# Performance work log

Hardware: AMD Instinct MI355X
Metric: run time of the kernel (lower is better)

## Reference

```python
import jax, jax.numpy as jnp
import numpy as np

H = 256  # hidden_size


def setup_inputs() -> dict:
    key = jax.random.key(0)
    ks = jax.random.split(key, 9)
    std = 1.0 / np.sqrt(H)
    u = lambda k, shape: jax.random.uniform(k, shape, jnp.float32, -std, std)
    x = jax.random.normal(ks[0], (64, 16, 128, 64), jnp.float32)
    return {
        "x": x,
        "wi0": u(ks[1], (64, 3 * H)),
        "wh0": u(ks[2], (H, 3 * H)),
        "bi0": u(ks[3], (3 * H,)),
        "bh0": u(ks[4], (3 * H,)),
        "wi1": u(ks[5], (H, 3 * H)),
        "wh1": u(ks[6], (H, 3 * H)),
        "bi1": u(ks[7], (3 * H,)),
        "bh1": u(ks[8], (3 * H,)),
    }


def _cell(x_t, h, wi, wh, bi, bh):
    # x_t: (B, N, D), h: (B, N, H). Gates concatenated as [r|z|n].
    gi = x_t @ wi + bi           # (B, N, 3H)
    gh = h @ wh + bh             # (B, N, 3H)
    ir, iz, inn = jnp.split(gi, 3, axis=-1)
    hr, hz, hn = jnp.split(gh, 3, axis=-1)
    r = jax.nn.sigmoid(ir + hr)
    z = jax.nn.sigmoid(iz + hz)
    n = jnp.tanh(inn + r * hn)
    return (1.0 - z) * n + z * h


def reference(x, wi0, wh0, bi0, bh0, wi1, wh1, bi1, bh1):
    seq_len, B, N, _ = x.shape
    h0 = jnp.zeros((B, N, H), x.dtype)
    h1 = jnp.zeros((B, N, H), x.dtype)

    def step(carry, x_t):
        h0, h1 = carry
        h0 = _cell(x_t, h0, wi0, wh0, bi0, bh0)
        h1 = _cell(h0, h1, wi1, wh1, bi1, bh1)
        return (h0, h1), h1

    (h0, h1), output = jax.lax.scan(step, (h0, h1), x)
    hidden_out = jnp.stack([h0, h1], axis=0)  # (num_layers, B, N, H)
    return output, hidden_out
```

## Files before the change

kernel.cpp:

```cpp
#include <hip/hip_runtime.h>


typedef __attribute__((ext_vector_type(8))) __bf16 bf8;
typedef __attribute__((ext_vector_type(8))) unsigned short u16x8;
typedef __attribute__((ext_vector_type(4))) float f32x4;

#define MFMA16(A, B, C) __builtin_amdgcn_mfma_f32_16x16x32_bf16((A), (B), (C), 0, 0, 0)

#define ROWS 2048
#define HID 256
#define NW 768
#define SLOT (ROWS * HID)
#define OUT_HID_OFF ((size_t)64 * ROWS * HID)

#define WI1_OFF 0
#define WH1_OFF 12288

static __device__ __forceinline__ float b2f(unsigned short u) {
  union { unsigned u32; float f; } v;
  v.u32 = ((unsigned)u) << 16;
  return v.f;
}
static __device__ __forceinline__ unsigned short f2b(float f) {
  unsigned u = __float_as_uint(f);
  u += 0x7fffu + ((u >> 16) & 1u);
  return (unsigned short)(u >> 16);
}
static __device__ __forceinline__ float sigm(float x) {
  return 1.0f / (1.0f + __expf(-x));
}
static __device__ __forceinline__ float tanh_fast(float x) {
  x = fminf(15.0f, fmaxf(-15.0f, x));
  float e = __expf(2.0f * x);
  return (e - 1.0f) / (e + 1.0f);
}
static __device__ __forceinline__ float ldin(const void* p, int i, int f32w) {
  return f32w ? ((const float*)p)[i] : b2f(((const unsigned short*)p)[i]);
}
static __device__ __forceinline__ void stout(void* p, size_t i, float v, int f32w) {
  if (f32w) ((float*)p)[i] = v;
  else ((unsigned short*)p)[i] = f2b(v);
}

static __device__ __forceinline__ bf8 ld_h16(const unsigned short* p) {
  union { unsigned long long q[2]; bf8 b; } u;
  u.q[0] = __hip_atomic_load((const unsigned long long*)p, __ATOMIC_RELAXED,
                             __HIP_MEMORY_SCOPE_AGENT);
  u.q[1] = __hip_atomic_load((const unsigned long long*)(p + 4), __ATOMIC_RELAXED,
                             __HIP_MEMORY_SCOPE_AGENT);
  return u.b;
}
static __device__ __forceinline__ void st_h2(unsigned short* p, unsigned short v) {
  asm volatile("global_store_short %0, %1, off sc0 sc1"
               : : "v"(p), "v"((unsigned)v) : "memory");
}

__global__ void probe_dtype(const unsigned short* x, unsigned* flag) {
  if (blockIdx.x != 0 || threadIdx.x != 0) return;
  int cnt = 0;
  for (int i = 0; i < 256; ++i) {
    float v = b2f(x[i]);
    if (v == v && fabsf(v) <= 8.0f) cnt++;
  }
  *flag = (cnt >= 250) ? 0u : 1u;
}

__global__ void pack_w(const void* __restrict__ W,
                       unsigned short* __restrict__ P, int KK,
                       const unsigned* __restrict__ flag) {
  int i = blockIdx.x * blockDim.x + threadIdx.x;
  int total = 48 * KK * 64;
  if (i >= total) return;
  int f32w = (int)*flag;
  int l = i & 63;
  int kk = (i >> 6) % KK;
  int nb = i / (64 * KK);
  int n = nb * 16 + (l & 15);
  int k0 = kk * 32 + (l >> 4) * 8;
  u16x8 tmp;
#pragma unroll
  for (int e = 0; e < 8; ++e) tmp[e] = f2b(ldin(W, (k0 + e) * NW + n, f32w));
  *(u16x8*)(P + (size_t)i * 8) = tmp;
}

static __device__ __forceinline__ void gemm_x_bf16(
    const unsigned short* aBase, const unsigned short* xw, int lane,
    f32x4* aR, f32x4* aZ, f32x4* aT) {
#pragma unroll
  for (int kk = 0; kk < 2; ++kk) {
    bf8 A0 = *(const bf8*)(aBase + kk * 32);
    bf8 A1 = *(const bf8*)(aBase + 16 * 64 + kk * 32);
    const int lb = lane * 8;
    bf8 Br = *(const bf8*)(xw + 0 * 16384 + kk * 512 + lb);
    bf8 Bz = *(const bf8*)(xw + 1 * 16384 + kk * 512 + lb);
    bf8 Bn = *(const bf8*)(xw + 2 * 16384 + kk * 512 + lb);
    aR[0] = MFMA16(A0, Br, aR[0]);
    aR[1] = MFMA16(A1, Br, aR[1]);
    aZ[0] = MFMA16(A0, Bz, aZ[0]);
    aZ[1] = MFMA16(A1, Bz, aZ[1]);
    aT[0] = MFMA16(A0, Bn, aT[0]);
    aT[1] = MFMA16(A1, Bn, aT[1]);
  }
}
static __device__ __forceinline__ void gemm_x_f32(
    const float* aBase, const unsigned short* xw, int lane,
    f32x4* aR, f32x4* aZ, f32x4* aT) {
#pragma unroll
  for (int kk = 0; kk < 2; ++kk) {
    union { u16x8 u; bf8 b; } A0, A1;
#pragma unroll
    for (int e = 0; e < 8; ++e) {
      A0.u[e] = f2b(aBase[kk * 32 + e]);
      A1.u[e] = f2b(aBase[16 * 64 + kk * 32 + e]);
    }
    const int lb = lane * 8;
    bf8 Br = *(const bf8*)(xw + 0 * 16384 + kk * 512 + lb);
    bf8 Bz = *(const bf8*)(xw + 1 * 16384 + kk * 512 + lb);
    bf8 Bn = *(const bf8*)(xw + 2 * 16384 + kk * 512 + lb);
    aR[0] = MFMA16(A0.b, Br, aR[0]);
    aR[1] = MFMA16(A1.b, Br, aR[1]);
    aZ[0] = MFMA16(A0.b, Bz, aZ[0]);
    aZ[1] = MFMA16(A1.b, Bz, aZ[1]);
    aT[0] = MFMA16(A0.b, Bn, aT[0]);
    aT[1] = MFMA16(A1.b, Bn, aT[1]);
  }
}
static __device__ __forceinline__ void gemm_h0(
    const unsigned short* aBase, const unsigned short* w0,
    const unsigned short* smem, int lane,
    f32x4* aR0, f32x4* aZ0, f32x4* aH0,
    f32x4* aR1, f32x4* aZ1, f32x4* aI1) {
#pragma unroll
  for (int kk = 0; kk < 8; ++kk) {
    bf8 A0 = ld_h16(aBase + kk * 32);
    bf8 A1 = ld_h16(aBase + 16 * HID + kk * 32);
    const int lb = lane * 8;
    bf8 Br0 = *(const bf8*)(w0 + 0 * 65536 + kk * 512 + lb);
    bf8 Bz0 = *(const bf8*)(w0 + 1 * 65536 + kk * 512 + lb);
    bf8 Bn0 = *(const bf8*)(w0 + 2 * 65536 + kk * 512 + lb);
    bf8 Br1 = *(const bf8*)(smem + WI1_OFF + (0 * 8 + kk) * 512 + lb);
    bf8 Bz1 = *(const bf8*)(smem + WI1_OFF + (1 * 8 + kk) * 512 + lb);
    bf8 Bn1 = *(const bf8*)(smem + WI1_OFF + (2 * 8 + kk) * 512 + lb);
    aR0[0] = MFMA16(A0, Br0, aR0[0]);
    aR0[1] = MFMA16(A1, Br0, aR0[1]);
    aZ0[0] = MFMA16(A0, Bz0, aZ0[0]);
    aZ0[1] = MFMA16(A1, Bz0, aZ0[1]);
    aH0[0] = MFMA16(A0, Bn0, aH0[0]);
    aH0[1] = MFMA16(A1, Bn0, aH0[1]);
    aR1[0] = MFMA16(A0, Br1, aR1[0]);
    aR1[1] = MFMA16(A1, Br1, aR1[1]);
    aZ1[0] = MFMA16(A0, Bz1, aZ1[0]);
    aZ1[1] = MFMA16(A1, Bz1, aZ1[1]);
    aI1[0] = MFMA16(A0, Bn1, aI1[0]);
    aI1[1] = MFMA16(A1, Bn1, aI1[1]);
  }
}
static __device__ __forceinline__ void gemm_h1(
    const unsigned short* aBase, const unsigned short* smem, int lane,
    f32x4* aR, f32x4* aZ, f32x4* aH) {
#pragma unroll
  for (int kk = 0; kk < 8; ++kk) {
    bf8 A0 = ld_h16(aBase + kk * 32);
    bf8 A1 = ld_h16(aBase + 16 * HID + kk * 32);
    const int lb = lane * 8;
    bf8 Br = *(const bf8*)(smem + WH1_OFF + (0 * 8 + kk) * 512 + lb);
    bf8 Bz = *(const bf8*)(smem + WH1_OFF + (1 * 8 + kk) * 512 + lb);
    bf8 Bn = *(const bf8*)(smem + WH1_OFF + (2 * 8 + kk) * 512 + lb);
    aR[0] = MFMA16(A0, Br, aR[0]);
    aR[1] = MFMA16(A1, Br, aR[1]);
    aZ[0] = MFMA16(A0, Bz, aZ[0]);
    aZ[1] = MFMA16(A1, Bz, aZ[1]);
    aH[0] = MFMA16(A0, Bn, aH[0]);
    aH[1] = MFMA16(A1, Bn, aH[1]);
  }
}

__global__ void __launch_bounds__(256, 1) gru_main(
    const void* __restrict__ x,
    const void* __restrict__ bi0, const void* __restrict__ bh0,
    const void* __restrict__ bi1, const void* __restrict__ bh1,
    const unsigned short* __restrict__ pwi0, const unsigned short* __restrict__ pwh0,
    const unsigned short* __restrict__ pwi1, const unsigned short* __restrict__ pwh1,
    void* __restrict__ out,
    unsigned short* __restrict__ h0b, unsigned short* __restrict__ h1b,
    unsigned* __restrict__ flags, const unsigned* __restrict__ flag) {
  __shared__ __align__(16) unsigned short smem[24576];

  const int f32w = (int)*flag;
  const int tid = threadIdx.x;
  const int lane = tid & 63;
  const int wid = tid >> 6;
  const int bid = blockIdx.x;
  const int g = bid & 15;
  const int slice = bid >> 4;

  const int d = slice * 16 + (lane & 15);
  const int rb = g * 128 + wid * 32;
  const int arow = rb + (lane & 15);
  const int koff = (lane >> 4) * 8;
  const int rl = (lane >> 4) * 4;

  unsigned* flagp = flags + (size_t)g * 64;

  for (int i = tid; i < 1536; i += 256) {
    int gg = i >> 9, r = i & 511;
    *(u16x8*)(smem + WI1_OFF + gg * 4096 + r * 8) =
        *(const u16x8*)(pwi1 + (size_t)(gg * 16 + slice) * 4096 + r * 8);
    *(u16x8*)(smem + WH1_OFF + gg * 4096 + r * 8) =
        *(const u16x8*)(pwh1 + (size_t)(gg * 16 + slice) * 4096 + r * 8);
  }
  __syncthreads();

  const unsigned short* xw = pwi0 + (size_t)slice * 1024;
  const unsigned short* w0 = pwh0 + (size_t)slice * 4096;

  const float iR0 = ldin(bi0, d, f32w) + ldin(bh0, d, f32w);
  const float iZ0 = ldin(bi0, 256 + d, f32w) + ldin(bh0, 256 + d, f32w);
  const float iI0 = ldin(bi0, 512 + d, f32w);
  const float iH0 = ldin(bh0, 512 + d, f32w);
  const float iR1 = ldin(bi1, d, f32w) + ldin(bh1, d, f32w);
  const float iZ1 = ldin(bi1, 256 + d, f32w) + ldin(bh1, 256 + d, f32w);
  const float iI1 = ldin(bi1, 512 + d, f32w);
  const float iH1 = ldin(bh1, 512 + d, f32w);

  float h0p[2][4] = {{0, 0, 0, 0}, {0, 0, 0, 0}};
  float h1p[2][4] = {{0, 0, 0, 0}, {0, 0, 0, 0}};

  for (int t = 0; t <= 64; ++t) {
    const int sc = t & 1;
    const int sp = sc ^ 1;

    f32x4 aR0[2], aZ0[2], aI0[2], aH0[2], aR1[2], aZ1[2], aI1[2], aH1[2];
#pragma unroll
    for (int f = 0; f < 2; ++f) {
      aR0[f] = (f32x4){iR0, iR0, iR0, iR0};
      aZ0[f] = (f32x4){iZ0, iZ0, iZ0, iZ0};
      aI0[f] = (f32x4){iI0, iI0, iI0, iI0};
      aH0[f] = (f32x4){iH0, iH0, iH0, iH0};
      aR1[f] = (f32x4){iR1, iR1, iR1, iR1};
      aZ1[f] = (f32x4){iZ1, iZ1, iZ1, iZ1};
      aI1[f] = (f32x4){iI1, iI1, iI1, iI1};
      aH1[f] = (f32x4){iH1, iH1, iH1, iH1};
    }

    if (t < 64) {
      size_t xoff = ((size_t)t * ROWS + arow) * 64 + koff;
      if (f32w) gemm_x_f32((const float*)x + xoff, xw, lane, aR0, aZ0, aI0);
      else gemm_x_bf16((const unsigned short*)x + xoff, xw, lane, aR0, aZ0, aI0);
    }

    if (t > 0) {
      if (tid == 0) {
        const unsigned tgt = 16u * (unsigned)t;
        while (__hip_atomic_load(flagp, __ATOMIC_RELAXED,
                                 __HIP_MEMORY_SCOPE_AGENT) < tgt)
          __builtin_amdgcn_s_sleep(1);
      }
      __syncthreads();
    }

    gemm_h0(h0b + (size_t)sp * SLOT + (size_t)arow * HID + koff, w0, smem,
            lane, aR0, aZ0, aH0, aR1, aZ1, aI1);
    if (t >= 2)
      gemm_h1(h1b + (size_t)sc * SLOT + (size_t)arow * HID + koff, smem, lane,
              aR1, aZ1, aH1);

    if (t < 64) {
#pragma unroll
      for (int f = 0; f < 2; ++f) {
#pragma unroll
        for (int j = 0; j < 4; ++j) {
          int row = rb + f * 16 + rl + j;
          float r = sigm(aR0[f][j]);
          float z = sigm(aZ0[f][j]);
          float n = tanh_fast(aI0[f][j] + r * aH0[f][j]);
          float hv = (1.0f - z) * n + z * h0p[f][j];
          h0p[f][j] = hv;
          st_h2(h0b + (size_t)sc * SLOT + (size_t)row * HID + d, f2b(hv));
          if (t == 63) stout(out, OUT_HID_OFF + (size_t)row * HID + d, hv, f32w);
        }
      }
    }
    if (t >= 1) {
      const int tm1 = t - 1;
#pragma unroll
      for (int f = 0; f < 2; ++f) {
#pragma unroll
        for (int j = 0; j < 4; ++j) {
          int row = rb + f * 16 + rl + j;
          float r = sigm(aR1[f][j]);
          float z = sigm(aZ1[f][j]);
          float n = tanh_fast(aI1[f][j] + r * aH1[f][j]);
          float hv = (1.0f - z) * n + z * h1p[f][j];
          h1p[f][j] = hv;
          st_h2(h1b + (size_t)sp * SLOT + (size_t)row * HID + d, f2b(hv));
          stout(out, ((size_t)tm1 * ROWS + row) * HID + d, hv, f32w);
          if (tm1 == 63)
            stout(out, OUT_HID_OFF + (size_t)SLOT + (size_t)row * HID + d, hv, f32w);
        }
      }
    }

    asm volatile("s_waitcnt vmcnt(0)" ::: "memory");
    __syncthreads();
    if (t < 64 && tid == 0)
      __hip_atomic_fetch_add(flagp, 1u, __ATOMIC_RELAXED, __HIP_MEMORY_SCOPE_AGENT);
  }
}

extern "C" void kernel_launch(void* const* d_in, const int* in_sizes, int n_in,
                              void* d_out, int out_size, void* d_ws, size_t ws_size,
                              hipStream_t stream) {
  (void)in_sizes; (void)n_in; (void)out_size; (void)ws_size;
  const void* x   = d_in[0];
  const void* wi0 = d_in[1];
  const void* wh0 = d_in[2];
  const void* bi0 = d_in[3];
  const void* bh0 = d_in[4];
  const void* wi1 = d_in[5];
  const void* wh1 = d_in[6];
  const void* bi1 = d_in[7];
  const void* bh1 = d_in[8];
  void* out = d_out;

  char* ws = (char*)d_ws;
  unsigned* flags = (unsigned*)ws;
  unsigned* flag  = (unsigned*)(ws + 4096);
  unsigned short* h0b = (unsigned short*)(ws + 8192);
  unsigned short* h1b = (unsigned short*)(ws + 8192 + 2097152);
  unsigned short* pwi0 = (unsigned short*)(ws + 8192 + 4194304);
  unsigned short* pwh0 = pwi0 + 49152;
  unsigned short* pwi1 = pwh0 + 196608;
  unsigned short* pwh1 = pwi1 + 196608;

  hipMemsetAsync(d_ws, 0, 8192 + 2097152, stream);

  probe_dtype<<<1, 64, 0, stream>>>((const unsigned short*)x, flag);

  pack_w<<<(48 * 2 * 64 + 255) / 256, 256, 0, stream>>>(wi0, pwi0, 2, flag);
  pack_w<<<(48 * 8 * 64 + 255) / 256, 256, 0, stream>>>(wh0, pwh0, 8, flag);
  pack_w<<<(48 * 8 * 64 + 255) / 256, 256, 0, stream>>>(wi1, pwi1, 8, flag);
  pack_w<<<(48 * 8 * 64 + 255) / 256, 256, 0, stream>>>(wh1, pwh1, 8, flag);

  void* kargs[] = {&x, &bi0, &bh0, &bi1, &bh1, &pwi0, &pwh0, &pwi1, &pwh1,
                   &out, &h0b, &h1b, &flags, &flag};
  hipError_t lerr = hipLaunchCooperativeKernel(
      (const void*)gru_main, dim3(256), dim3(256), kargs, 0, stream);
  if (lerr != hipSuccess) {
    (void)hipGetLastError();
    gru_main<<<dim3(256), dim3(256), 0, stream>>>(
        x, bi0, bh0, bi1, bh1, pwi0, pwh0, pwi1, pwh1,
        out, h0b, h1b, flags, flag);
  }
}
```

Measured before the change: 793.3 us.

## Per-wave flag synchronization, hoist h loads, defer output stores past signal

Replaces the block-wide __syncthreads handshake with per-wave polling and per-wave flag increments (target becomes 64 per step), so each wavefront proceeds independently across time steps. Hidden-state A operands for both layers are loaded up front into register arrays before the MFMA chains, to overlap load latency. Output stores are moved after the completion signal so they stay off the critical recurrence path, and the memory clobber on the h store asm is dropped. The trade-offs are higher register pressure and more atomic traffic, and dropping the clobber risks the compiler reordering memory operations around those stores.

```diff
diff --git a/kernel.cpp b/kernel.cpp
--- a/kernel.cpp
+++ b/kernel.cpp
@@ -52,7 +52,7 @@
 }
 static __device__ __forceinline__ void st_h2(unsigned short* p, unsigned short v) {
   asm volatile("global_store_short %0, %1, off sc0 sc1"
-               : : "v"(p), "v"((unsigned)v) : "memory");
+               : : "v"(p), "v"((unsigned)v));
 }
 
 __global__ void probe_dtype(const unsigned short* x, unsigned* flag) {
@@ -125,55 +125,6 @@
     aT[1] = MFMA16(A1.b, Bn, aT[1]);
   }
 }
-static __device__ __forceinline__ void gemm_h0(
-    const unsigned short* aBase, const unsigned short* w0,
-    const unsigned short* smem, int lane,
-    f32x4* aR0, f32x4* aZ0, f32x4* aH0,
-    f32x4* aR1, f32x4* aZ1, f32x4* aI1) {
-#pragma unroll
-  for (int kk = 0; kk < 8; ++kk) {
-    bf8 A0 = ld_h16(aBase + kk * 32);
-    bf8 A1 = ld_h16(aBase + 16 * HID + kk * 32);
-    const int lb = lane * 8;
-    bf8 Br0 = *(const bf8*)(w0 + 0 * 65536 + kk * 512 + lb);
-    bf8 Bz0 = *(const bf8*)(w0 + 1 * 65536 + kk * 512 + lb);
-    bf8 Bn0 = *(const bf8*)(w0 + 2 * 65536 + kk * 512 + lb);
-    bf8 Br1 = *(const bf8*)(smem + WI1_OFF + (0 * 8 + kk) * 512 + lb);
-    bf8 Bz1 = *(const bf8*)(smem + WI1_OFF + (1 * 8 + kk) * 512 + lb);
-    bf8 Bn1 = *(const bf8*)(smem + WI1_OFF + (2 * 8 + kk) * 512 + lb);
-    aR0[0] = MFMA16(A0, Br0, aR0[0]);
-    aR0[1] = MFMA16(A1, Br0, aR0[1]);
-    aZ0[0] = MFMA16(A0, Bz0, aZ0[0]);
-    aZ0[1] = MFMA16(A1, Bz0, aZ0[1]);
-    aH0[0] = MFMA16(A0, Bn0, aH0[0]);
-    aH0[1] = MFMA16(A1, Bn0, aH0[1]);
-    aR1[0] = MFMA16(A0, Br1, aR1[0]);
-    aR1[1] = MFMA16(A1, Br1, aR1[1]);
-    aZ1[0] = MFMA16(A0, Bz1, aZ1[0]);
-    aZ1[1] = MFMA16(A1, Bz1, aZ1[1]);
-    aI1[0] = MFMA16(A0, Bn1, aI1[0]);
-    aI1[1] = MFMA16(A1, Bn1, aI1[1]);
-  }
-}
-static __device__ __forceinline__ void gemm_h1(
-    const unsigned short* aBase, const unsigned short* smem, int lane,
-    f32x4* aR, f32x4* aZ, f32x4* aH) {
-#pragma unroll
-  for (int kk = 0; kk < 8; ++kk) {
-    bf8 A0 = ld_h16(aBase + kk * 32);
-    bf8 A1 = ld_h16(aBase + 16 * HID + kk * 32);
-    const int lb = lane * 8;
-    bf8 Br = *(const bf8*)(smem + WH1_OFF + (0 * 8 + kk) * 512 + lb);
-    bf8 Bz = *(const bf8*)(smem + WH1_OFF + (1 * 8 + kk) * 512 + lb);
-    bf8 Bn = *(const bf8*)(smem + WH1_OFF + (2 * 8 + kk) * 512 + lb);
-    aR[0] = MFMA16(A0, Br, aR[0]);
-    aR[1] = MFMA16(A1, Br, aR[1]);
-    aZ[0] = MFMA16(A0, Bz, aZ[0]);
-    aZ[1] = MFMA16(A1, Bz, aZ[1]);
-    aH[0] = MFMA16(A0, Bn, aH[0]);
-    aH[1] = MFMA16(A1, Bn, aH[1]);
-  }
-}
 
 __global__ void __launch_bounds__(256, 1) gru_main(
     const void* __restrict__ x,
@@ -250,20 +201,70 @@
     }
 
     if (t > 0) {
-      if (tid == 0) {
-        const unsigned tgt = 16u * (unsigned)t;
+      if (lane == 0) {
+        const unsigned tgt = 64u * (unsigned)t;
         while (__hip_atomic_load(flagp, __ATOMIC_RELAXED,
                                  __HIP_MEMORY_SCOPE_AGENT) < tgt)
           __builtin_amdgcn_s_sleep(1);
       }
-      __syncthreads();
-    }
-
-    gemm_h0(h0b + (size_t)sp * SLOT + (size_t)arow * HID + koff, w0, smem,
-            lane, aR0, aZ0, aH0, aR1, aZ1, aI1);
-    if (t >= 2)
-      gemm_h1(h1b + (size_t)sc * SLOT + (size_t)arow * HID + koff, smem, lane,
-              aR1, aZ1, aH1);
+      __builtin_amdgcn_sched_barrier(0);
+    }
+
+    const unsigned short* a0b =
+        h0b + (size_t)sp * SLOT + (size_t)arow * HID + koff;
+    bf8 A00[8], A01[8], A10[8], A11[8];
+#pragma unroll
+    for (int kk = 0; kk < 8; ++kk) {
+      A00[kk] = ld_h16(a0b + kk * 32);
+      A01[kk] = ld_h16(a0b + 16 * HID + kk * 32);
+    }
+    if (t >= 2) {
+      const unsigned short* a1b =
+          h1b + (size_t)sc * SLOT + (size_t)arow * HID + koff;
+#pragma unroll
+      for (int kk = 0; kk < 8; ++kk) {
+        A10[kk] = ld_h16(a1b + kk * 32);
+        A11[kk] = ld_h16(a1b + 16 * HID + kk * 32);
+      }
+    }
+
+#pragma unroll
+    for (int kk = 0; kk < 8; ++kk) {
+      const int lb = lane * 8;
+      bf8 Br0 = *(const bf8*)(w0 + 0 * 65536 + kk * 512 + lb);
+      bf8 Bz0 = *(const bf8*)(w0 + 1 * 65536 + kk * 512 + lb);
+      bf8 Bn0 = *(const bf8*)(w0 + 2 * 65536 + kk * 512 + lb);
+      bf8 Br1 = *(const bf8*)(smem + WI1_OFF + (0 * 8 + kk) * 512 + lb);
+      bf8 Bz1 = *(const bf8*)(smem + WI1_OFF + (1 * 8 + kk) * 512 + lb);
+      bf8 Bn1 = *(const bf8*)(smem + WI1_OFF + (2 * 8 + kk) * 512 + lb);
+      aR0[0] = MFMA16(A00[kk], Br0, aR0[0]);
+      aR0[1] = MFMA16(A01[kk], Br0, aR0[1]);
+      aZ0[0] = MFMA16(A00[kk], Bz0, aZ0[0]);
+      aZ0[1] = MFMA16(A01[kk], Bz0, aZ0[1]);
+      aH0[0] = MFMA16(A00[kk], Bn0, aH0[0]);
+      aH0[1] = MFMA16(A01[kk], Bn0, aH0[1]);
+      aR1[0] = MFMA16(A00[kk], Br1, aR1[0]);
+      aR1[1] = MFMA16(A01[kk], Br1, aR1[1]);
+      aZ1[0] = MFMA16(A00[kk], Bz1, aZ1[0]);
+      aZ1[1] = MFMA16(A01[kk], Bz1, aZ1[1]);
+      aI1[0] = MFMA16(A00[kk], Bn1, aI1[0]);
+      aI1[1] = MFMA16(A01[kk], Bn1, aI1[1]);
+    }
+    if (t >= 2) {
+#pragma unroll
+      for (int kk = 0; kk < 8; ++kk) {
+        const int lb = lane * 8;
+        bf8 Br = *(const bf8*)(smem + WH1_OFF + (0 * 8 + kk) * 512 + lb);
+        bf8 Bz = *(const bf8*)(smem + WH1_OFF + (1 * 8 + kk) * 512 + lb);
+        bf8 Bn = *(const bf8*)(smem + WH1_OFF + (2 * 8 + kk) * 512 + lb);
+        aR1[0] = MFMA16(A10[kk], Br, aR1[0]);
+        aR1[1] = MFMA16(A11[kk], Br, aR1[1]);
+        aZ1[0] = MFMA16(A10[kk], Bz, aZ1[0]);
+        aZ1[1] = MFMA16(A11[kk], Bz, aZ1[1]);
+        aH1[0] = MFMA16(A10[kk], Bn, aH1[0]);
+        aH1[1] = MFMA16(A11[kk], Bn, aH1[1]);
+      }
+    }
 
     if (t < 64) {
 #pragma unroll
@@ -277,12 +278,10 @@
           float hv = (1.0f - z) * n + z * h0p[f][j];
           h0p[f][j] = hv;
           st_h2(h0b + (size_t)sc * SLOT + (size_t)row * HID + d, f2b(hv));
-          if (t == 63) stout(out, OUT_HID_OFF + (size_t)row * HID + d, hv, f32w);
         }
       }
     }
     if (t >= 1) {
-      const int tm1 = t - 1;
 #pragma unroll
       for (int f = 0; f < 2; ++f) {
 #pragma unroll
@@ -294,17 +293,39 @@
           float hv = (1.0f - z) * n + z * h1p[f][j];
           h1p[f][j] = hv;
           st_h2(h1b + (size_t)sp * SLOT + (size_t)row * HID + d, f2b(hv));
-          stout(out, ((size_t)tm1 * ROWS + row) * HID + d, hv, f32w);
+        }
+      }
+    }
+
+    asm volatile("s_waitcnt vmcnt(0)" ::: "memory");
+    if (t < 64 && lane == 0)
+      __hip_atomic_fetch_add(flagp, 1u, __ATOMIC_RELAXED,
+                             __HIP_MEMORY_SCOPE_AGENT);
+
+    if (t >= 1) {
+      const int tm1 = t - 1;
+#pragma unroll
+      for (int f = 0; f < 2; ++f) {
+#pragma unroll
+        for (int j = 0; j < 4; ++j) {
+          int row = rb + f * 16 + rl + j;
+          stout(out, ((size_t)tm1 * ROWS + row) * HID + d, h1p[f][j], f32w);
           if (tm1 == 63)
-            stout(out, OUT_HID_OFF + (size_t)SLOT + (size_t)row * HID + d, hv, f32w);
+            stout(out, OUT_HID_OFF + (size_t)SLOT + (size_t)row * HID + d,
+                  h1p[f][j], f32w);
         }
       }
     }
-
-    asm volatile("s_waitcnt vmcnt(0)" ::: "memory");
-    __syncthreads();
-    if (t < 64 && tid == 0)
-      __hip_atomic_fetch_add(flagp, 1u, __ATOMIC_RELAXED, __HIP_MEMORY_SCOPE_AGENT);
+    if (t == 63) {
+#pragma unroll
+      for (int f = 0; f < 2; ++f) {
+#pragma unroll
+        for (int j = 0; j < 4; ++j) {
+          int row = rb + f * 16 + rl + j;
+          stout(out, OUT_HID_OFF + (size_t)row * HID + d, h0p[f][j], f32w);
+        }
+      }
+    }
   }
 }
 
```

Measured after the change: 854.5 us. 7.7% more time.
